# Kernel tuning notes

Hardware: AMD Instinct MI355X
Metric: run time of the kernel (lower is better)

The kernel has to match this reference:

```python
import jax, jax.numpy as jnp
import numpy as np

E, D, DFF = 8, 1024, 4096

def setup_inputs() -> dict:
    key = jax.random.key(0)
    ks = jax.random.split(key, 10)
    s = 0.02
    return {
        "x":  jax.random.normal(ks[0], (4, 2048, D), dtype=jnp.float32),
        "Wr": jax.random.normal(ks[1], (D, E), dtype=jnp.float32) * s,
        "br": jnp.zeros((E,), dtype=jnp.float32),
        "W1": jax.random.normal(ks[2], (E, D, DFF), dtype=jnp.float32) * s,
        "b1": jnp.zeros((E, DFF), dtype=jnp.float32),
        "W2": jax.random.normal(ks[3], (E, D, DFF), dtype=jnp.float32) * s,
        "b2": jnp.zeros((E, DFF), dtype=jnp.float32),
        "W3": jax.random.normal(ks[4], (E, DFF, D), dtype=jnp.float32) * s,
        "b3": jnp.zeros((E, D), dtype=jnp.float32),
    }

def reference(x, Wr, br, W1, b1, W2, b2, W3, b3):
    b, s, d = x.shape
    xt = x.reshape(b * s, d)                       # [T, D]
    logits = xt @ Wr + br                          # [T, E]
    pr, idx = jax.lax.top_k(logits, 2)             # [T, 2]
    w = jax.nn.softmax(pr, axis=-1)                # softmax over the 2 selected experts
    # combine weight per (token, expert): sum of routing weights where expert selected
    onehot = jax.nn.one_hot(idx, W1.shape[0], dtype=x.dtype)  # [T, 2, E]
    cw = jnp.einsum('tk,tke->te', w, onehot)       # [T, E]
    y = jnp.zeros_like(xt)
    for e in range(W1.shape[0]):                   # small fixed expert loop
        h = jax.nn.silu(xt @ W1[e] + b1[e]) * (xt @ W2[e] + b2[e])  # SwiGLU [T, DFF]
        y = y + (h @ W3[e] + b3[e]) * cw[:, e:e + 1]
    return y.reshape(b, s, d)
```

## Files before the change

kernel.cpp:

```cpp
#include <hip/hip_runtime.h>

#define T_TOK 8192
#define DIM   1024
#define DFF_  4096
#define NE    8
#define MAXT  144

typedef float  f32x4 __attribute__((ext_vector_type(4)));
typedef __bf16 b16x8 __attribute__((ext_vector_type(8)));
typedef unsigned short u16x4 __attribute__((ext_vector_type(4)));

__device__ __forceinline__ unsigned short f2bf(float f) {
  union { float f; unsigned int u; } v; v.f = f;
  unsigned int r = v.u + 0x7fffu + ((v.u >> 16) & 1u);
  return (unsigned short)(r >> 16);
}

__device__ __forceinline__ void gload_lds16(const void* g, void* l) {
  __builtin_amdgcn_global_load_lds((const __attribute__((address_space(1))) void*)g,
                                   (__attribute__((address_space(3))) void*)l,
                                   16, 0, 0);
}

#define DRAIN_VMCNT() asm volatile("s_waitcnt vmcnt(0)" ::: "memory")

__global__ __launch_bounds__(256) void transpose_cvt(const float* __restrict__ src,
                                                     unsigned short* __restrict__ dst,
                                                     int R, int C) {
  __shared__ float tile[64][68];
  size_t mat = (size_t)blockIdx.z * R * C;
  int c0 = blockIdx.x * 64, r0 = blockIdx.y * 64;
  int t = threadIdx.x;
  int rcol = (t & 15) * 4, rrow = t >> 4;
  const float* s = src + mat + (size_t)r0 * C + c0;
#pragma unroll
  for (int i = 0; i < 4; i++) {
    int r = rrow + i * 16;
    f32x4 v = *(const f32x4*)(s + (size_t)r * C + rcol);
    *(f32x4*)(&tile[r][rcol]) = v;
  }
  __syncthreads();
  unsigned short* d = dst + mat + (size_t)c0 * R + r0;
  int wrow4 = (t & 15) * 4, wcol = t >> 4;
#pragma unroll
  for (int i = 0; i < 4; i++) {
    int cc = wcol + i * 16;
    u16x4 o;
    o[0] = f2bf(tile[wrow4 + 0][cc]);
    o[1] = f2bf(tile[wrow4 + 1][cc]);
    o[2] = f2bf(tile[wrow4 + 2][cc]);
    o[3] = f2bf(tile[wrow4 + 3][cc]);
    *(u16x4*)(&d[(size_t)cc * R + wrow4]) = o;
  }
}

__global__ __launch_bounds__(256) void router_k(const float* __restrict__ x,
                                                const float* __restrict__ Wr,
                                                const float* __restrict__ br,
                                                unsigned short* __restrict__ Xbf,
                                                int* __restrict__ top2e,
                                                float* __restrict__ top2w,
                                                int* __restrict__ counts) {
  __shared__ int lcnt[NE];
  if (threadIdx.x < NE) lcnt[threadIdx.x] = 0;
  __syncthreads();
  int wid = threadIdx.x >> 6, lane = threadIdx.x & 63;
  int t = blockIdx.x * 4 + wid;
  const float* xr = x + (size_t)t * DIM;
  unsigned short* xb = Xbf + (size_t)t * DIM;
  float s[NE];
#pragma unroll
  for (int e = 0; e < NE; e++) s[e] = 0.f;
  for (int i = 0; i < DIM / 64; i++) {
    int dd = i * 64 + lane;
    float xv = xr[dd];
    xb[dd] = f2bf(xv);
    const float* w = Wr + (size_t)dd * NE;
#pragma unroll
    for (int e = 0; e < NE; e++) s[e] += xv * w[e];
  }
#pragma unroll
  for (int m = 32; m >= 1; m >>= 1) {
#pragma unroll
    for (int e = 0; e < NE; e++) s[e] += __shfl_xor(s[e], m, 64);
  }
  if (lane == 0) {
#pragma unroll
    for (int e = 0; e < NE; e++) s[e] += br[e];
    int e0 = 0;
#pragma unroll
    for (int e = 1; e < NE; e++) if (s[e] > s[e0]) e0 = e;
    int e1 = (e0 == 0) ? 1 : 0;
#pragma unroll
    for (int e = 0; e < NE; e++) if (e != e0 && s[e] > s[e1]) e1 = e;
    float w0 = 1.f / (1.f + expf(s[e1] - s[e0]));
    top2e[2 * t] = e0; top2e[2 * t + 1] = e1;
    top2w[2 * t] = w0; top2w[2 * t + 1] = 1.f - w0;
    atomicAdd(&lcnt[e0], 1);
    atomicAdd(&lcnt[e1], 1);
  }
  __syncthreads();
  if (threadIdx.x < NE) atomicAdd(&counts[threadIdx.x], lcnt[threadIdx.x]);
}

__global__ void scan_build(int* __restrict__ ctrl) {
  if (threadIdx.x != 0 || blockIdx.x != 0) return;
  int* counts = ctrl;
  int* offsets = ctrl + 8;
  int* cursors = ctrl + 16;
  int* nt256 = ctrl + 24;
  int* tE256 = ctrl + 32;
  int* tM256 = ctrl + 32 + MAXT;
  int o = 0;
  for (int e = 0; e < NE; e++) { offsets[e] = o; cursors[e] = o; o += counts[e]; }
  int a = 0;
  for (int e = 0; e < NE; e++)
    for (int m0 = 0; m0 < counts[e]; m0 += 256) { tE256[a] = e; tM256[a] = m0; a++; }
  nt256[0] = a;
}

__global__ __launch_bounds__(256) void scatter_k(const int* __restrict__ top2e,
                                                 const float* __restrict__ top2w,
                                                 int* __restrict__ cursors,
                                                 int* __restrict__ list_tok,
                                                 float* __restrict__ list_w) {
  __shared__ int lcnt[NE];
  __shared__ int lbase[NE];
  int tid = threadIdx.x;
  if (tid < NE) lcnt[tid] = 0;
  __syncthreads();
  int t = blockIdx.x * 256 + tid;
  int e0 = top2e[2 * t], e1 = top2e[2 * t + 1];
  int r0 = atomicAdd(&lcnt[e0], 1);
  int r1 = atomicAdd(&lcnt[e1], 1);
  __syncthreads();
  if (tid < NE) lbase[tid] = atomicAdd(&cursors[tid], lcnt[tid]);
  __syncthreads();
  int p0 = lbase[e0] + r0, p1 = lbase[e1] + r1;
  list_tok[p0] = t; list_w[p0] = top2w[2 * t];
  list_tok[p1] = t; list_w[p1] = top2w[2 * t + 1];
}

__global__ __launch_bounds__(1024, 4) void gemm1_k(const unsigned short* __restrict__ Xbf,
                                                   const unsigned short* __restrict__ W1T,
                                                   const unsigned short* __restrict__ W2T,
                                                   const float* __restrict__ b1,
                                                   const float* __restrict__ b2,
                                                   unsigned short* __restrict__ H,
                                                   const int* __restrict__ list_tok,
                                                   const int* __restrict__ ctrl) {
  const int* counts = ctrl; const int* offsets = ctrl + 8;
  const int* ntile = ctrl + 24;
  const int* tileE = ctrl + 32; const int* tileM = ctrl + 32 + MAXT;
  int bt = blockIdx.y;
  if (bt >= ntile[0]) return;
  int e = tileE[bt], m0 = tileM[bt];
  int Me = counts[e], off = offsets[e];
  int n0 = blockIdx.x * 128;

  __shared__ unsigned short lds[2][32768];

  int tid = threadIdx.x, lane = tid & 63, wid = tid >> 6;
  int wr = wid >> 2, wc = wid & 3;

  const unsigned short* gsrc[4];
  unsigned ldsoff[4];
  {
    int lr = lane >> 3;
    int sc = ((lane & 7) ^ (lane >> 3)) * 8;
#pragma unroll
    for (int j = 0; j < 4; j++) {
      int c = wid * 4 + j;
      ldsoff[j] = c * 512;
      if (c < 32) {
        int r = c * 8 + lr;
        int tok = (m0 + r < Me) ? list_tok[off + m0 + r] : list_tok[off];
        gsrc[j] = Xbf + (size_t)tok * DIM + sc;
      } else if (c < 48) {
        int n = n0 + (c - 32) * 8 + lr;
        gsrc[j] = W1T + ((size_t)e * DFF_ + n) * DIM + sc;
      } else {
        int n = n0 + (c - 48) * 8 + lr;
        gsrc[j] = W2T + ((size_t)e * DFF_ + n) * DIM + sc;
      }
    }
  }

  unsigned aoff[2][4], boff[2][2];
  {
    int colg = lane >> 4;
#pragma unroll
    for (int kk = 0; kk < 2; kk++) {
#pragma unroll
      for (int m = 0; m < 4; m++) {
        int row = wr * 64 + m * 16 + (lane & 15);
        aoff[kk][m] = row * 64 + (((kk * 4 + colg) ^ (row & 7)) * 8);
      }
#pragma unroll
      for (int n = 0; n < 2; n++) {
        int row = wc * 32 + n * 16 + (lane & 15);
        boff[kk][n] = 16384 + row * 64 + (((kk * 4 + colg) ^ (row & 7)) * 8);
      }
    }
  }

  f32x4 acc1[4][2], acc2[4][2];
#pragma unroll
  for (int i = 0; i < 4; i++)
#pragma unroll
    for (int j = 0; j < 2; j++) {
      acc1[i][j] = f32x4{0.f, 0.f, 0.f, 0.f};
      acc2[i][j] = f32x4{0.f, 0.f, 0.f, 0.f};
    }

  auto compute = [&](const unsigned short* base) {
#pragma unroll
    for (int kk = 0; kk < 2; kk++) {
      b16x8 aF[4], bF1[2], bF2[2];
#pragma unroll
      for (int m = 0; m < 4; m++) aF[m] = *(const b16x8*)(base + aoff[kk][m]);
#pragma unroll
      for (int n = 0; n < 2; n++) {
        bF1[n] = *(const b16x8*)(base + boff[kk][n]);
        bF2[n] = *(const b16x8*)(base + boff[kk][n] + 8192);
      }
#pragma unroll
      for (int m = 0; m < 4; m++)
#pragma unroll
        for (int n = 0; n < 2; n++) {
          acc1[m][n] = __builtin_amdgcn_mfma_f32_16x16x32_bf16(aF[m], bF1[n], acc1[m][n], 0, 0, 0);
          acc2[m][n] = __builtin_amdgcn_mfma_f32_16x16x32_bf16(aF[m], bF2[n], acc2[m][n], 0, 0, 0);
        }
    }
  };

#pragma unroll
  for (int j = 0; j < 4; j++) gload_lds16(gsrc[j], (void*)(&lds[0][ldsoff[j]]));
  DRAIN_VMCNT();
  __syncthreads();

  int cur = 0;
  const int NK = DIM / 64;
  for (int kt = 0; kt < NK; kt++) {
    if (kt + 1 < NK) {
#pragma unroll
      for (int j = 0; j < 4; j++)
        gload_lds16(gsrc[j] + (kt + 1) * 64, (void*)(&lds[cur ^ 1][ldsoff[j]]));
    }
    compute(&lds[cur][0]);
    DRAIN_VMCNT();
    __syncthreads();
    cur ^= 1;
  }

#pragma unroll
  for (int n = 0; n < 2; n++) {
    int col = n0 + wc * 32 + n * 16 + (lane & 15);
    float bb1 = b1[e * DFF_ + col], bb2 = b2[e * DFF_ + col];
#pragma unroll
    for (int m = 0; m < 4; m++) {
      int rbase = wr * 64 + m * 16 + (lane >> 4) * 4;
#pragma unroll
      for (int r = 0; r < 4; r++) {
        int rr = rbase + r;
        if (m0 + rr < Me) {
          float c1 = acc1[m][n][r] + bb1;
          float c2 = acc2[m][n][r] + bb2;
          float h = c1 * c2 / (1.f + __expf(-c1));
          H[(size_t)(off + m0 + rr) * DFF_ + col] = f2bf(h);
        }
      }
    }
  }
}

__global__ __launch_bounds__(1024, 4) void gemm2_k(const unsigned short* __restrict__ H,
                                                   const unsigned short* __restrict__ W3T,
                                                   const float* __restrict__ b3,
                                                   const int* __restrict__ list_tok,
                                                   const float* __restrict__ list_w,
                                                   float* __restrict__ y,
                                                   const int* __restrict__ ctrl) {
  const int* counts = ctrl; const int* offsets = ctrl + 8;
  const int* ntile = ctrl + 24;
  const int* tileE = ctrl + 32; const int* tileM = ctrl + 32 + MAXT;
  int bt = blockIdx.y;
  if (bt >= ntile[0]) return;
  int e = tileE[bt], m0 = tileM[bt];
  int Me = counts[e], off = offsets[e];
  int n0 = blockIdx.x * 256;

  __shared__ unsigned short lds[2][32768];

  int tid = threadIdx.x, lane = tid & 63, wid = tid >> 6;
  int wr = wid >> 2, wc = wid & 3;

  const unsigned short* gsrc[4];
  unsigned ldsoff[4];
  {
    int lr = lane >> 3;
    int sc = ((lane & 7) ^ (lane >> 3)) * 8;
#pragma unroll
    for (int j = 0; j < 4; j++) {
      int c = wid * 4 + j;
      ldsoff[j] = c * 512;
      if (c < 32) {
        int r = c * 8 + lr;
        int pos = (m0 + r < Me) ? (off + m0 + r) : off;
        gsrc[j] = H + (size_t)pos * DFF_ + sc;
      } else {
        int n = n0 + (c - 32) * 8 + lr;
        gsrc[j] = W3T + ((size_t)e * DIM + n) * DFF_ + sc;
      }
    }
  }

  unsigned aoff[2][4], boff[2][4];
  {
    int colg = lane >> 4;
#pragma unroll
    for (int kk = 0; kk < 2; kk++) {
#pragma unroll
      for (int m = 0; m < 4; m++) {
        int row = wr * 64 + m * 16 + (lane & 15);
        aoff[kk][m] = row * 64 + (((kk * 4 + colg) ^ (row & 7)) * 8);
      }
#pragma unroll
      for (int n = 0; n < 4; n++) {
        int row = wc * 64 + n * 16 + (lane & 15);
        boff[kk][n] = 16384 + row * 64 + (((kk * 4 + colg) ^ (row & 7)) * 8);
      }
    }
  }

  f32x4 acc[4][4];
#pragma unroll
  for (int i = 0; i < 4; i++)
#pragma unroll
    for (int j = 0; j < 4; j++) acc[i][j] = f32x4{0.f, 0.f, 0.f, 0.f};

  auto compute = [&](const unsigned short* base) {
#pragma unroll
    for (int kk = 0; kk < 2; kk++) {
      b16x8 aF[4], bF[4];
#pragma unroll
      for (int m = 0; m < 4; m++) aF[m] = *(const b16x8*)(base + aoff[kk][m]);
#pragma unroll
      for (int n = 0; n < 4; n++) bF[n] = *(const b16x8*)(base + boff[kk][n]);
#pragma unroll
      for (int m = 0; m < 4; m++)
#pragma unroll
        for (int n = 0; n < 4; n++)
          acc[m][n] = __builtin_amdgcn_mfma_f32_16x16x32_bf16(aF[m], bF[n], acc[m][n], 0, 0, 0);
    }
  };

#pragma unroll
  for (int j = 0; j < 4; j++) gload_lds16(gsrc[j], (void*)(&lds[0][ldsoff[j]]));
  DRAIN_VMCNT();
  __syncthreads();

  int cur = 0;
  const int NK = DFF_ / 64;
  for (int kt = 0; kt < NK; kt++) {
    if (kt + 1 < NK) {
#pragma unroll
      for (int j = 0; j < 4; j++)
        gload_lds16(gsrc[j] + (kt + 1) * 64, (void*)(&lds[cur ^ 1][ldsoff[j]]));
    }
    compute(&lds[cur][0]);
    DRAIN_VMCNT();
    __syncthreads();
    cur ^= 1;
  }

#pragma unroll
  for (int n = 0; n < 4; n++) {
    int col = n0 + wc * 64 + n * 16 + (lane & 15);
    float bb3 = b3[e * DIM + col];
#pragma unroll
    for (int m = 0; m < 4; m++) {
      int rbase = wr * 64 + m * 16 + (lane >> 4) * 4;
#pragma unroll
      for (int r = 0; r < 4; r++) {
        int rr = rbase + r;
        if (m0 + rr < Me) {
          int pos = off + m0 + rr;
          float v = list_w[pos] * (acc[m][n][r] + bb3);
          atomicAdd(&y[(size_t)list_tok[pos] * DIM + col], v);
        }
      }
    }
  }
}

extern "C" void kernel_launch(void* const* d_in, const int* in_sizes, int n_in,
                              void* d_out, int out_size, void* d_ws, size_t ws_size,
                              hipStream_t stream) {
  (void)in_sizes; (void)n_in; (void)ws_size;
  const float* x  = (const float*)d_in[0];
  const float* Wr = (const float*)d_in[1];
  const float* br = (const float*)d_in[2];
  const float* W1 = (const float*)d_in[3];
  const float* b1 = (const float*)d_in[4];
  const float* W2 = (const float*)d_in[5];
  const float* b2 = (const float*)d_in[6];
  const float* W3 = (const float*)d_in[7];
  const float* b3 = (const float*)d_in[8];
  float* y = (float*)d_out;
  char* ws = (char*)d_ws;

  const size_t matB = (size_t)NE * DFF_ * DIM * 2;
  size_t oW1T = 0;
  size_t oW2T = oW1T + matB;
  size_t oXbf = oW2T + matB;
  size_t oH   = oXbf + (size_t)T_TOK * DIM * 2;
  size_t oT2e = oH + (size_t)2 * T_TOK * DFF_ * 2;
  size_t oT2w = oT2e + (size_t)2 * T_TOK * 4;
  size_t oLtk = oT2w + (size_t)2 * T_TOK * 4;
  size_t oLw  = oLtk + (size_t)2 * T_TOK * 4;
  size_t oCtl = oLw + (size_t)2 * T_TOK * 4;

  unsigned short* W1T = (unsigned short*)(ws + oW1T);
  unsigned short* W2T = (unsigned short*)(ws + oW2T);
  unsigned short* W3T = (unsigned short*)(ws + oW1T);
  unsigned short* Xbf = (unsigned short*)(ws + oXbf);
  unsigned short* Hb  = (unsigned short*)(ws + oH);
  int*   top2e = (int*)(ws + oT2e);
  float* top2w = (float*)(ws + oT2w);
  int*   ltok  = (int*)(ws + oLtk);
  float* lw    = (float*)(ws + oLw);
  int*   ctrl  = (int*)(ws + oCtl);

  hipMemsetAsync(y, 0, (size_t)out_size * 4, stream);
  hipMemsetAsync(ctrl, 0, (32 + 2 * MAXT) * 4, stream);

  transpose_cvt<<<dim3(DFF_ / 64, DIM / 64, NE), 256, 0, stream>>>(W1, W1T, DIM, DFF_);
  transpose_cvt<<<dim3(DFF_ / 64, DIM / 64, NE), 256, 0, stream>>>(W2, W2T, DIM, DFF_);
  router_k<<<dim3(T_TOK / 4), 256, 0, stream>>>(x, Wr, br, Xbf, top2e, top2w, ctrl);
  scan_build<<<dim3(1), 64, 0, stream>>>(ctrl);
  scatter_k<<<dim3(T_TOK / 256), 256, 0, stream>>>(top2e, top2w, ctrl + 16, ltok, lw);
  gemm1_k<<<dim3(DFF_ / 128, 71), 1024, 0, stream>>>(Xbf, W1T, W2T, b1, b2, Hb, ltok, ctrl);
  transpose_cvt<<<dim3(DIM / 64, DFF_ / 64, NE), 256, 0, stream>>>(W3, W3T, DFF_, DIM);
  gemm2_k<<<dim3(DIM / 256, 71), 1024, 0, stream>>>(Hb, W3T, b3, ltok, lw, y, ctrl);
}
```

Before: 706.7 us.

## Deepen gemm1 LDS pipeline to four K=32 stages with partial waitcnt

The gemm1 mainloop changes from a double-buffered K=64 tile with a full vmcnt drain each step to a four-stage ring of K=32 tiles. Each step waits on a partial vmcnt so up to three loads stay in flight. MFMA blocks are wrapped in s_setprio, and the LDS swizzle is adjusted for 32-wide rows. The transpose kernel now uses an XOR-swizzled LDS tile with 8-wide bf16 stores, and the router reads x with vectorized float4 loads. The gain comes from better overlap of global loads with compute. The cost is two barriers per smaller K step and reliance on correct vmcnt accounting.

```diff
diff --git a/kernel.cpp b/kernel.cpp
--- a/kernel.cpp
+++ b/kernel.cpp
@@ -9,6 +9,7 @@
 typedef float  f32x4 __attribute__((ext_vector_type(4)));
 typedef __bf16 b16x8 __attribute__((ext_vector_type(8)));
 typedef unsigned short u16x4 __attribute__((ext_vector_type(4)));
+typedef unsigned short u16x8 __attribute__((ext_vector_type(8)));
 
 __device__ __forceinline__ unsigned short f2bf(float f) {
   union { float f; unsigned int u; } v; v.f = f;
@@ -22,35 +23,41 @@
                                    16, 0, 0);
 }
 
+#define WAITCNT(n) asm volatile("s_waitcnt vmcnt(" #n ")" ::: "memory")
 #define DRAIN_VMCNT() asm volatile("s_waitcnt vmcnt(0)" ::: "memory")
+#define SBAR() do { asm volatile("" ::: "memory"); __builtin_amdgcn_s_barrier(); \
+                    asm volatile("" ::: "memory"); } while (0)
 
 __global__ __launch_bounds__(256) void transpose_cvt(const float* __restrict__ src,
                                                      unsigned short* __restrict__ dst,
                                                      int R, int C) {
-  __shared__ float tile[64][68];
+  __shared__ float tile[64 * 64];
   size_t mat = (size_t)blockIdx.z * R * C;
   int c0 = blockIdx.x * 64, r0 = blockIdx.y * 64;
   int t = threadIdx.x;
-  int rcol = (t & 15) * 4, rrow = t >> 4;
   const float* s = src + mat + (size_t)r0 * C + c0;
+  int rrow = t >> 4, c4r = t & 15;
 #pragma unroll
   for (int i = 0; i < 4; i++) {
     int r = rrow + i * 16;
-    f32x4 v = *(const f32x4*)(s + (size_t)r * C + rcol);
-    *(f32x4*)(&tile[r][rcol]) = v;
+    f32x4 v = *(const f32x4*)(s + (size_t)r * C + c4r * 4);
+    int c4s = c4r ^ (r >> 3);
+    *(f32x4*)(&tile[r * 64 + c4s * 4]) = v;
   }
   __syncthreads();
   unsigned short* d = dst + mat + (size_t)c0 * R + r0;
-  int wrow4 = (t & 15) * 4, wcol = t >> 4;
-#pragma unroll
-  for (int i = 0; i < 4; i++) {
-    int cc = wcol + i * 16;
-    u16x4 o;
-    o[0] = f2bf(tile[wrow4 + 0][cc]);
-    o[1] = f2bf(tile[wrow4 + 1][cc]);
-    o[2] = f2bf(tile[wrow4 + 2][cc]);
-    o[3] = f2bf(tile[wrow4 + 3][cc]);
-    *(u16x4*)(&d[(size_t)cc * R + wrow4]) = o;
+  int wr8 = (t & 7) * 8, wcol = t >> 3;
+#pragma unroll
+  for (int i = 0; i < 2; i++) {
+    int cc = wcol + i * 32;
+    u16x8 o;
+#pragma unroll
+    for (int j = 0; j < 8; j++) {
+      int r = wr8 + j;
+      int c4 = (cc >> 2) ^ (r >> 3);
+      o[j] = f2bf(tile[r * 64 + c4 * 4 + (cc & 3)]);
+    }
+    *(u16x8*)(&d[(size_t)cc * R + wr8]) = o;
   }
 }
 
@@ -71,13 +78,19 @@
   float s[NE];
 #pragma unroll
   for (int e = 0; e < NE; e++) s[e] = 0.f;
-  for (int i = 0; i < DIM / 64; i++) {
-    int dd = i * 64 + lane;
-    float xv = xr[dd];
-    xb[dd] = f2bf(xv);
-    const float* w = Wr + (size_t)dd * NE;
-#pragma unroll
-    for (int e = 0; e < NE; e++) s[e] += xv * w[e];
+  for (int i = 0; i < DIM / 256; i++) {
+    int dd = i * 256 + lane * 4;
+    f32x4 xv = *(const f32x4*)(xr + dd);
+    u16x4 xb4;
+#pragma unroll
+    for (int j = 0; j < 4; j++) xb4[j] = f2bf(xv[j]);
+    *(u16x4*)(&xb[dd]) = xb4;
+#pragma unroll
+    for (int j = 0; j < 4; j++) {
+      const float* w = Wr + (size_t)(dd + j) * NE;
+#pragma unroll
+      for (int e = 0; e < NE; e++) s[e] += xv[j] * w[e];
+    }
   }
 #pragma unroll
   for (int m = 32; m >= 1; m >>= 1) {
@@ -158,49 +171,46 @@
   int Me = counts[e], off = offsets[e];
   int n0 = blockIdx.x * 128;
 
-  __shared__ unsigned short lds[2][32768];
+  __shared__ unsigned short lds[4][16384];
 
   int tid = threadIdx.x, lane = tid & 63, wid = tid >> 6;
   int wr = wid >> 2, wc = wid & 3;
 
-  const unsigned short* gsrc[4];
-  unsigned ldsoff[4];
+  const unsigned short* gsrc[2];
+  unsigned ldsoff[2];
   {
-    int lr = lane >> 3;
-    int sc = ((lane & 7) ^ (lane >> 3)) * 8;
-#pragma unroll
-    for (int j = 0; j < 4; j++) {
-      int c = wid * 4 + j;
+    int lr = lane >> 2;
+    int sc = ((lane & 3) ^ ((lane >> 3) & 3)) * 8;
+#pragma unroll
+    for (int j = 0; j < 2; j++) {
+      int c = wid * 2 + j;
       ldsoff[j] = c * 512;
-      if (c < 32) {
-        int r = c * 8 + lr;
+      if (c < 16) {
+        int r = c * 16 + lr;
         int tok = (m0 + r < Me) ? list_tok[off + m0 + r] : list_tok[off];
         gsrc[j] = Xbf + (size_t)tok * DIM + sc;
-      } else if (c < 48) {
-        int n = n0 + (c - 32) * 8 + lr;
+      } else if (c < 24) {
+        int n = n0 + (c - 16) * 16 + lr;
         gsrc[j] = W1T + ((size_t)e * DFF_ + n) * DIM + sc;
       } else {
-        int n = n0 + (c - 48) * 8 + lr;
+        int n = n0 + (c - 24) * 16 + lr;
         gsrc[j] = W2T + ((size_t)e * DFF_ + n) * DIM + sc;
       }
     }
   }
 
-  unsigned aoff[2][4], boff[2][2];
+  unsigned aoff[4], boff[2];
   {
     int colg = lane >> 4;
 #pragma unroll
-    for (int kk = 0; kk < 2; kk++) {
-#pragma unroll
-      for (int m = 0; m < 4; m++) {
-        int row = wr * 64 + m * 16 + (lane & 15);
-        aoff[kk][m] = row * 64 + (((kk * 4 + colg) ^ (row & 7)) * 8);
-      }
-#pragma unroll
-      for (int n = 0; n < 2; n++) {
-        int row = wc * 32 + n * 16 + (lane & 15);
-        boff[kk][n] = 16384 + row * 64 + (((kk * 4 + colg) ^ (row & 7)) * 8);
-      }
+    for (int m = 0; m < 4; m++) {
+      int row = wr * 64 + m * 16 + (lane & 15);
+      aoff[m] = row * 32 + ((colg ^ ((row >> 1) & 3)) * 8);
+    }
+#pragma unroll
+    for (int n = 0; n < 2; n++) {
+      int row = wc * 32 + n * 16 + (lane & 15);
+      boff[n] = 8192 + row * 32 + ((colg ^ ((row >> 1) & 3)) * 8);
     }
   }
 
@@ -213,45 +223,45 @@
       acc2[i][j] = f32x4{0.f, 0.f, 0.f, 0.f};
     }
 
-  auto compute = [&](const unsigned short* base) {
-#pragma unroll
-    for (int kk = 0; kk < 2; kk++) {
-      b16x8 aF[4], bF1[2], bF2[2];
-#pragma unroll
-      for (int m = 0; m < 4; m++) aF[m] = *(const b16x8*)(base + aoff[kk][m]);
+  auto compute16 = [&](const unsigned short* base) {
+    b16x8 aF[4], bF1[2], bF2[2];
+#pragma unroll
+    for (int m = 0; m < 4; m++) aF[m] = *(const b16x8*)(base + aoff[m]);
+#pragma unroll
+    for (int n = 0; n < 2; n++) {
+      bF1[n] = *(const b16x8*)(base + boff[n]);
+      bF2[n] = *(const b16x8*)(base + boff[n] + 4096);
+    }
+    __builtin_amdgcn_s_setprio(1);
+#pragma unroll
+    for (int m = 0; m < 4; m++)
 #pragma unroll
       for (int n = 0; n < 2; n++) {
-        bF1[n] = *(const b16x8*)(base + boff[kk][n]);
-        bF2[n] = *(const b16x8*)(base + boff[kk][n] + 8192);
-      }
-#pragma unroll
-      for (int m = 0; m < 4; m++)
-#pragma unroll
-        for (int n = 0; n < 2; n++) {
-          acc1[m][n] = __builtin_amdgcn_mfma_f32_16x16x32_bf16(aF[m], bF1[n], acc1[m][n], 0, 0, 0);
-          acc2[m][n] = __builtin_amdgcn_mfma_f32_16x16x32_bf16(aF[m], bF2[n], acc2[m][n], 0, 0, 0);
-        }
-    }
+        acc1[m][n] = __builtin_amdgcn_mfma_f32_16x16x32_bf16(aF[m], bF1[n], acc1[m][n], 0, 0, 0);
+        acc2[m][n] = __builtin_amdgcn_mfma_f32_16x16x32_bf16(aF[m], bF2[n], acc2[m][n], 0, 0, 0);
+      }
+    __builtin_amdgcn_s_setprio(0);
   };
 
-#pragma unroll
-  for (int j = 0; j < 4; j++) gload_lds16(gsrc[j], (void*)(&lds[0][ldsoff[j]]));
-  DRAIN_VMCNT();
-  __syncthreads();
-
-  int cur = 0;
-  const int NK = DIM / 64;
-  for (int kt = 0; kt < NK; kt++) {
-    if (kt + 1 < NK) {
-#pragma unroll
-      for (int j = 0; j < 4; j++)
-        gload_lds16(gsrc[j] + (kt + 1) * 64, (void*)(&lds[cur ^ 1][ldsoff[j]]));
-    }
-    compute(&lds[cur][0]);
-    DRAIN_VMCNT();
-    __syncthreads();
-    cur ^= 1;
-  }
+  const int NS = DIM / 32;
+#pragma unroll
+  for (int sp = 0; sp < 3; sp++)
+#pragma unroll
+    for (int j = 0; j < 2; j++)
+      gload_lds16(gsrc[j] + sp * 32, (void*)(&lds[sp][ldsoff[j]]));
+
+  for (int s = 0; s < NS - 3; s++) {
+    unsigned short* pb = &lds[(s + 3) & 3][0];
+    gload_lds16(gsrc[0] + (s + 3) * 32, (void*)(pb + ldsoff[0]));
+    gload_lds16(gsrc[1] + (s + 3) * 32, (void*)(pb + ldsoff[1]));
+    WAITCNT(6);
+    SBAR();
+    compute16(&lds[s & 3][0]);
+    SBAR();
+  }
+  WAITCNT(4); SBAR(); compute16(&lds[(NS - 3) & 3][0]);
+  WAITCNT(2); SBAR(); compute16(&lds[(NS - 2) & 3][0]);
+  WAITCNT(0); SBAR(); compute16(&lds[(NS - 1) & 3][0]);
 
 #pragma unroll
   for (int n = 0; n < 2; n++) {
```

Result: slower. 753.5 us (+6.6%).
